# Performance work log

Hardware: AMD Instinct MI355X
Metric: run time of the kernel (lower is better)

The kernel has to match this reference:

```python
import jax, jax.numpy as jnp
import numpy as np

ALPHA = 1.0  # init alpha


def setup_inputs() -> dict:
    key = jax.random.key(0)
    X = jax.random.normal(key, (4096, 512), dtype=jnp.float32)
    return {"X": X}


def reference(X):
    # Pairwise squared L2 distances via GEMM expansion:
    # ||x_i - x_j||^2 = ||x_i||^2 + ||x_j||^2 - 2 x_i . x_j
    # (same math as ((X[None]-X[:,None])**2).sum(-1) without the O(N^2 D) blow-up)
    sq = jnp.sum(X * X, axis=1)                      # [N]
    d2 = sq[:, None] + sq[None, :] - 2.0 * (X @ X.T)  # [N, N]
    # track_running_stats=True: sigma^2 = alpha * mean(d2), detached in torch
    sigma_square = ALPHA * jax.lax.stop_gradient(jnp.mean(d2))
    return jnp.exp(-d2 / (2.0 * sigma_square))
```

## Files before the change

kernel.cpp:

```cpp
#include <hip/hip_runtime.h>
#include <cstdint>

typedef unsigned short u16;
typedef unsigned int u32;
typedef __bf16 bf16x8 __attribute__((ext_vector_type(8)));
typedef float f32x4 __attribute__((ext_vector_type(4)));

#define N_ROWS 4096
#define D_COLS 512

__device__ __forceinline__ u16 f2bf(float f) {
    u32 u = __float_as_uint(f);
    u += 0x7fffu + ((u >> 16) & 1u);
    return (u16)(u >> 16);
}

#define GLDS(g, l)                                                            \
    __builtin_amdgcn_global_load_lds(                                         \
        (const __attribute__((address_space(1))) void*)(g),                   \
        (__attribute__((address_space(3))) void*)(l), 16, 0, 0)

__global__ __launch_bounds__(256) void k_prep(const float* __restrict__ X,
                                              u16* __restrict__ Xb,
                                              float* __restrict__ sq,
                                              float* __restrict__ partial) {
    __shared__ float cs[4][512];
    const int tid = threadIdx.x;
    const int w = tid >> 6, l = tid & 63;
    const int row0 = blockIdx.x * 16 + w * 4;
    float csum[8] = {0.f,0.f,0.f,0.f,0.f,0.f,0.f,0.f};
#pragma unroll
    for (int r = 0; r < 4; ++r) {
        const int row = row0 + r;
        const float4* src = (const float4*)(X + (size_t)row * D_COLS);
        float4 f0 = src[l * 2];
        float4 f1 = src[l * 2 + 1];
        float v[8] = {f0.x, f0.y, f0.z, f0.w, f1.x, f1.y, f1.z, f1.w};
        float ss = 0.f;
#pragma unroll
        for (int j = 0; j < 8; ++j) { ss += v[j] * v[j]; csum[j] += v[j]; }
        uint4 st;
        st.x = (u32)f2bf(v[0]) | ((u32)f2bf(v[1]) << 16);
        st.y = (u32)f2bf(v[2]) | ((u32)f2bf(v[3]) << 16);
        st.z = (u32)f2bf(v[4]) | ((u32)f2bf(v[5]) << 16);
        st.w = (u32)f2bf(v[6]) | ((u32)f2bf(v[7]) << 16);
        *(uint4*)(Xb + (size_t)row * D_COLS + l * 8) = st;
#pragma unroll
        for (int m = 32; m > 0; m >>= 1) ss += __shfl_xor(ss, m, 64);
        if (l == 0) sq[row] = ss;
    }
#pragma unroll
    for (int j = 0; j < 8; ++j) cs[w][l * 8 + j] = csum[j];
    __syncthreads();
    for (int d = tid; d < 512; d += 256)
        partial[blockIdx.x * 512 + d] = cs[0][d] + cs[1][d] + cs[2][d] + cs[3][d];
}

__global__ __launch_bounds__(256) void k_sigma(const float* __restrict__ sq,
                                               const float* __restrict__ partial,
                                               float* __restrict__ parts) {
    __shared__ float csm[4][64];
    __shared__ float red[8];
    const int g = blockIdx.x;
    const int t = threadIdx.x;
    const int c = g * 64 + (t & 63);
    const int ch = t >> 6;
    float cssum = 0.f;
#pragma unroll 8
    for (int b = ch * 64; b < ch * 64 + 64; ++b) cssum += partial[b * 512 + c];
    csm[ch][t & 63] = cssum;
    float s1 = sq[g * 512 + t] + sq[g * 512 + 256 + t];
    __syncthreads();
    float s2 = 0.f;
    if (t < 64) {
        float v = csm[0][t] + csm[1][t] + csm[2][t] + csm[3][t];
        s2 = v * v;
    }
#pragma unroll
    for (int m = 32; m > 0; m >>= 1) {
        s1 += __shfl_xor(s1, m, 64);
        s2 += __shfl_xor(s2, m, 64);
    }
    if ((t & 63) == 0) { red[ch] = s1; red[4 + ch] = s2; }
    __syncthreads();
    if (t == 0) {
        parts[g] = red[0] + red[1] + red[2] + red[3];
        parts[8 + g] = red[4];
    }
}

__global__ __launch_bounds__(256, 3) void k_gemm(const u16* __restrict__ Xb,
                                                 const float* __restrict__ sq,
                                                 const float* __restrict__ parts,
                                                 float* __restrict__ out) {
    __shared__ __align__(16) u16 As[3][128 * 32];
    __shared__ __align__(16) u16 Bs[3][128 * 32];
    __shared__ float sqA[128], sqB[128];
    __shared__ float c_sh;

    const int tid = threadIdx.x;
    const int lane = tid & 63;
    const int wid = tid >> 6;
    const int wr = wid >> 1, wc = wid & 1;

    const int bid = blockIdx.x;
    const int xcd = bid & 7, rr = bid >> 3;
    const int by = (xcd >> 2) * 16 + (rr & 15);
    const int bx = (xcd & 3) * 8 + (rr >> 4);
    const int i0 = by * 128, j0 = bx * 128;

    if (tid < 128) sqA[tid] = sq[i0 + tid];
    else           sqB[tid - 128] = sq[j0 + tid - 128];
    if (tid == 0) {
        float S1 = 0.f, S2 = 0.f;
#pragma unroll
        for (int i = 0; i < 8; ++i) { S1 += parts[i]; S2 += parts[8 + i]; }
        const float mean_d2 = 2.f * S1 / (float)N_ROWS
                            - 2.f * S2 / ((float)N_ROWS * (float)N_ROWS);
        c_sh = -1.4426950408889634f / (2.f * mean_d2);
    }

    const int sr = tid >> 2;
    const int sby = (tid & 3) * 16;
    const int sw0 = sby ^ (((sr >> 1) & 3) << 4);
    const int sw1 = sby ^ ((((sr + 64) >> 1) & 3) << 4);
    const char* xb = (const char*)Xb;
    const char* gA0 = xb + (size_t)(i0 + sr) * 1024 + sw0;
    const char* gA1 = xb + (size_t)(i0 + sr + 64) * 1024 + sw1;
    const char* gB0 = xb + (size_t)(j0 + sr) * 1024 + sw0;
    const char* gB1 = xb + (size_t)(j0 + sr + 64) * 1024 + sw1;

#define STAGE(buf, kt)                                                        \
    do {                                                                      \
        GLDS(gA0 + (kt) * 64, (char*)As[buf] + tid * 16);                     \
        GLDS(gA1 + (kt) * 64, (char*)As[buf] + 4096 + tid * 16);              \
        GLDS(gB0 + (kt) * 64, (char*)Bs[buf] + tid * 16);                     \
        GLDS(gB1 + (kt) * 64, (char*)Bs[buf] + 4096 + tid * 16);              \
    } while (0)

    f32x4 acc[4][4];
#pragma unroll
    for (int m = 0; m < 4; ++m)
#pragma unroll
        for (int n = 0; n < 4; ++n) acc[m][n] = (f32x4){0.f, 0.f, 0.f, 0.f};

    const int frow = lane & 15;
    const int klane = lane >> 4;

    STAGE(0, 0);
    STAGE(1, 1);

    int cb = 0, nb = 2;
    for (int kt = 0; kt < 16; ++kt) {
        if (kt < 15) asm volatile("s_waitcnt vmcnt(4)" ::: "memory");
        else         asm volatile("s_waitcnt vmcnt(0)" ::: "memory");
        asm volatile("s_barrier" ::: "memory");
        if (kt + 2 < 16) STAGE(nb, kt + 2);
        const char* Ab = (const char*)As[cb];
        const char* Bb = (const char*)Bs[cb];
        bf16x8 a[4], b[4];
#pragma unroll
        for (int m = 0; m < 4; ++m) {
            const int row = wr * 64 + m * 16 + frow;
            a[m] = *(const bf16x8*)(Ab + row * 64 +
                                    ((klane * 16) ^ (((row >> 1) & 3) << 4)));
        }
#pragma unroll
        for (int n = 0; n < 4; ++n) {
            const int row = wc * 64 + n * 16 + frow;
            b[n] = *(const bf16x8*)(Bb + row * 64 +
                                    ((klane * 16) ^ (((row >> 1) & 3) << 4)));
        }
        __builtin_amdgcn_s_setprio(1);
#pragma unroll
        for (int m = 0; m < 4; ++m)
#pragma unroll
            for (int n = 0; n < 4; ++n)
                acc[m][n] = __builtin_amdgcn_mfma_f32_16x16x32_bf16(
                    a[m], b[n], acc[m][n], 0, 0, 0);
        __builtin_amdgcn_s_setprio(0);
        cb = (cb == 2) ? 0 : cb + 1;
        nb = (nb == 2) ? 0 : nb + 1;
    }
#undef STAGE

    const float cval = c_sh;
    const int q = lane >> 4;
#pragma unroll
    for (int m = 0; m < 4; ++m) {
#pragma unroll
        for (int n = 0; n < 4; ++n) {
            const int col = wc * 64 + n * 16 + frow;
            const float sb = sqB[col];
#pragma unroll
            for (int r = 0; r < 4; ++r) {
                const int row = wr * 64 + m * 16 + q * 4 + r;
                const float d2 = sqA[row] + sb - 2.0f * acc[m][n][r];
                __builtin_nontemporal_store(
                    exp2f(cval * d2),
                    &out[(size_t)(i0 + row) * N_ROWS + (j0 + col)]);
            }
        }
    }
}

extern "C" void kernel_launch(void* const* d_in, const int* in_sizes, int n_in,
                              void* d_out, int out_size, void* d_ws, size_t ws_size,
                              hipStream_t stream) {
    const float* X = (const float*)d_in[0];
    float* out = (float*)d_out;
    char* ws = (char*)d_ws;

    u16*   Xb   = (u16*)ws;
    float* part = (float*)(ws + (4u << 20));
    float* sq   = (float*)(ws + (4u << 20) + (512u << 10));
    float* prt  = (float*)(ws + (4u << 20) + (512u << 10) + (16u << 10));

    hipLaunchKernelGGL(k_prep, dim3(256), dim3(256), 0, stream, X, Xb, sq, part);
    hipLaunchKernelGGL(k_sigma, dim3(8), dim3(256), 0, stream, sq, part, prt);
    hipLaunchKernelGGL(k_gemm, dim3(1024), dim3(256), 0, stream, Xb, sq, prt, out);
}
```

Before: 53.38 us.

## Switch GEMM to double-buffered BK=64 tiles with XOR-swizzled LDS

Replaces the triple-buffered K=32 pipeline with a double-buffered K=64 pipeline, halving the number of k-iterations and barriers while doubling LDS per stage. It also changes the LDS swizzle to an 8-slot XOR and issues the first stage load before the sq and sigma setup. Block-to-XCD tile mapping is reshaped, and output stores become regular instead of nontemporal. Occupancy is lowered to 2 blocks per CU, and a full __syncthreads replaces vmcnt-based partial waits, which can expose load latency.

```diff
diff --git a/kernel.cpp b/kernel.cpp
--- a/kernel.cpp
+++ b/kernel.cpp
@@ -89,12 +89,12 @@
     }
 }
 
-__global__ __launch_bounds__(256, 3) void k_gemm(const u16* __restrict__ Xb,
+__global__ __launch_bounds__(256, 2) void k_gemm(const u16* __restrict__ Xb,
                                                  const float* __restrict__ sq,
                                                  const float* __restrict__ parts,
                                                  float* __restrict__ out) {
-    __shared__ __align__(16) u16 As[3][128 * 32];
-    __shared__ __align__(16) u16 Bs[3][128 * 32];
+    __shared__ __align__(16) u16 As[2][128 * 64];
+    __shared__ __align__(16) u16 Bs[2][128 * 64];
     __shared__ float sqA[128], sqB[128];
     __shared__ float c_sh;
 
@@ -105,10 +105,28 @@
 
     const int bid = blockIdx.x;
     const int xcd = bid & 7, rr = bid >> 3;
-    const int by = (xcd >> 2) * 16 + (rr & 15);
-    const int bx = (xcd & 3) * 8 + (rr >> 4);
+    const int by = (xcd >> 1) * 8 + (rr & 7);
+    const int bx = (xcd & 1) * 16 + (rr >> 3);
     const int i0 = by * 128, j0 = bx * 128;
 
+    const int strow = tid >> 3;
+    const int sslot = (tid & 7) ^ (strow & 7);
+    const char* xb = (const char*)Xb;
+    const char* gA = xb + (size_t)(i0 + strow) * 1024 + sslot * 16;
+    const char* gB = xb + (size_t)(j0 + strow) * 1024 + sslot * 16;
+
+#define STAGE(buf, kt)                                                        \
+    do {                                                                      \
+        _Pragma("unroll")                                                     \
+        for (int s = 0; s < 4; ++s) {                                         \
+            GLDS(gA + s * 32768 + (kt) * 128,                                 \
+                 (char*)As[buf] + s * 4096 + tid * 16);                       \
+            GLDS(gB + s * 32768 + (kt) * 128,                                 \
+                 (char*)Bs[buf] + s * 4096 + tid * 16);                       \
+        }                                                                     \
+    } while (0)
+
+    STAGE(0, 0);
     if (tid < 128) sqA[tid] = sq[i0 + tid];
     else           sqB[tid - 128] = sq[j0 + tid - 128];
     if (tid == 0) {
@@ -120,24 +138,6 @@
         c_sh = -1.4426950408889634f / (2.f * mean_d2);
     }
 
-    const int sr = tid >> 2;
-    const int sby = (tid & 3) * 16;
-    const int sw0 = sby ^ (((sr >> 1) & 3) << 4);
-    const int sw1 = sby ^ ((((sr + 64) >> 1) & 3) << 4);
-    const char* xb = (const char*)Xb;
-    const char* gA0 = xb + (size_t)(i0 + sr) * 1024 + sw0;
-    const char* gA1 = xb + (size_t)(i0 + sr + 64) * 1024 + sw1;
-    const char* gB0 = xb + (size_t)(j0 + sr) * 1024 + sw0;
-    const char* gB1 = xb + (size_t)(j0 + sr + 64) * 1024 + sw1;
-
-#define STAGE(buf, kt)                                                        \
-    do {                                                                      \
-        GLDS(gA0 + (kt) * 64, (char*)As[buf] + tid * 16);                     \
-        GLDS(gA1 + (kt) * 64, (char*)As[buf] + 4096 + tid * 16);              \
-        GLDS(gB0 + (kt) * 64, (char*)Bs[buf] + tid * 16);                     \
-        GLDS(gB1 + (kt) * 64, (char*)Bs[buf] + 4096 + tid * 16);              \
-    } while (0)
-
     f32x4 acc[4][4];
 #pragma unroll
     for (int m = 0; m < 4; ++m)
@@ -146,41 +146,33 @@
 
     const int frow = lane & 15;
     const int klane = lane >> 4;
-
-    STAGE(0, 0);
-    STAGE(1, 1);
-
-    int cb = 0, nb = 2;
-    for (int kt = 0; kt < 16; ++kt) {
-        if (kt < 15) asm volatile("s_waitcnt vmcnt(4)" ::: "memory");
-        else         asm volatile("s_waitcnt vmcnt(0)" ::: "memory");
-        asm volatile("s_barrier" ::: "memory");
-        if (kt + 2 < 16) STAGE(nb, kt + 2);
-        const char* Ab = (const char*)As[cb];
-        const char* Bb = (const char*)Bs[cb];
-        bf16x8 a[4], b[4];
-#pragma unroll
-        for (int m = 0; m < 4; ++m) {
-            const int row = wr * 64 + m * 16 + frow;
-            a[m] = *(const bf16x8*)(Ab + row * 64 +
-                                    ((klane * 16) ^ (((row >> 1) & 3) << 4)));
+    const int s0 = (klane ^ (frow & 7)) << 4;
+
+    for (int kt = 0; kt < 8; ++kt) {
+        const int buf = kt & 1;
+        __syncthreads();
+        if (kt < 7) STAGE(buf ^ 1, kt + 1);
+        const char* Ab = (const char*)As[buf];
+        const char* Bb = (const char*)Bs[buf];
+#pragma unroll
+        for (int ks = 0; ks < 2; ++ks) {
+            const int kb = s0 ^ (ks << 6);
+            bf16x8 a[4], b[4];
+#pragma unroll
+            for (int i = 0; i < 4; ++i)
+                a[i] = *(const bf16x8*)(Ab + (wr * 64 + i * 16 + frow) * 128 + kb);
+#pragma unroll
+            for (int n = 0; n < 4; ++n)
+                b[n] = *(const bf16x8*)(Bb + (wc * 64 + n * 16 + frow) * 128 + kb);
+            __builtin_amdgcn_s_setprio(1);
+#pragma unroll
+            for (int i = 0; i < 4; ++i)
+#pragma unroll
+                for (int n = 0; n < 4; ++n)
+                    acc[i][n] = __builtin_amdgcn_mfma_f32_16x16x32_bf16(
+                        a[i], b[n], acc[i][n], 0, 0, 0);
+            __builtin_amdgcn_s_setprio(0);
         }
-#pragma unroll
-        for (int n = 0; n < 4; ++n) {
-            const int row = wc * 64 + n * 16 + frow;
-            b[n] = *(const bf16x8*)(Bb + row * 64 +
-                                    ((klane * 16) ^ (((row >> 1) & 3) << 4)));
-        }
-        __builtin_amdgcn_s_setprio(1);
-#pragma unroll
-        for (int m = 0; m < 4; ++m)
-#pragma unroll
-            for (int n = 0; n < 4; ++n)
-                acc[m][n] = __builtin_amdgcn_mfma_f32_16x16x32_bf16(
-                    a[m], b[n], acc[m][n], 0, 0, 0);
-        __builtin_amdgcn_s_setprio(0);
-        cb = (cb == 2) ? 0 : cb + 1;
-        nb = (nb == 2) ? 0 : nb + 1;
     }
 #undef STAGE
 
@@ -196,9 +188,7 @@
             for (int r = 0; r < 4; ++r) {
                 const int row = wr * 64 + m * 16 + q * 4 + r;
                 const float d2 = sqA[row] + sb - 2.0f * acc[m][n][r];
-                __builtin_nontemporal_store(
-                    exp2f(cval * d2),
-                    &out[(size_t)(i0 + row) * N_ROWS + (j0 + col)]);
+                out[(size_t)(i0 + row) * N_ROWS + (j0 + col)] = exp2f(cval * d2);
             }
         }
     }
```

Result: faster. 45.99 us (-13.8%).
